# Optimization experiments

Hardware: AMD Instinct MI355X
Metric: run time of the kernel (lower is better)

Reference implementation:

```python
import jax, jax.numpy as jnp
import numpy as np

DIM_MODEL = 1024
NUM_HEADS = 16
DROPOUT_P = 0.5
SCALE = float(np.sqrt(DIM_MODEL // NUM_HEADS))  # NOTE: source MULTIPLIES by this (unusual but faithful)
DROP_KEY = jax.random.key(42)


def setup_inputs() -> dict:
    key = jax.random.key(0)
    ks = jax.random.split(key, 9)
    B, LQ, LK, D = 4, 2048, 2048, DIM_MODEL
    s = 1.0 / np.sqrt(D)
    return {
        "query": jax.random.normal(ks[0], (B, LQ, D), jnp.float32),
        "key": jax.random.normal(ks[1], (B, LK, D), jnp.float32),
        "value": jax.random.normal(ks[2], (B, LK, D), jnp.float32),
        "Wq": jax.random.normal(ks[3], (D, D), jnp.float32) * s,
        "bq": jax.random.normal(ks[4], (D,), jnp.float32) * s,
        "Wk": jax.random.normal(ks[5], (D, D), jnp.float32) * s,
        "bk": jax.random.normal(ks[6], (D,), jnp.float32) * s,
        "Wv": jax.random.normal(ks[7], (D, D), jnp.float32) * s,
        "bv": jax.random.normal(ks[8], (D,), jnp.float32) * s,
    }


def reference(query, key, value, Wq, bq, Wk, bk, Wv, bv):
    # Linear projections (W stored as [in, out])
    q = jnp.einsum('bqd,de->bqe', query, Wq) + bq
    k = jnp.einsum('bkd,de->bke', key, Wk) + bk
    v = jnp.einsum('bkd,de->bke', value, Wv) + bv
    # scores scaled by MULTIPLYING sqrt(d_head), per source
    scores = jnp.einsum('bqe,bke->bqk', q, k) * SCALE
    probs = jax.nn.softmax(scores, axis=-1)
    # dropout (train mode, p=0.5), deterministic fixed key for reproducibility
    keep = jax.random.bernoulli(DROP_KEY, 1.0 - DROPOUT_P, probs.shape)
    probs = jnp.where(keep, probs / (1.0 - DROPOUT_P), 0.0)
    return jnp.einsum('bqk,bke->bqe', probs, v)
```

## Files before the change

### kernel.cpp

```cpp
#include <hip/hip_runtime.h>
#include <math.h>

#define BATCH  4
#define LSEQ   2048
#define DMODEL 1024
#define MROWS  (BATCH * LSEQ)
#define SCORE_SCALE 8.0f

#define THREEFRY_PARTITIONABLE 1

typedef __bf16 bf16_t;
typedef bf16_t bf16x8 __attribute__((ext_vector_type(8)));
typedef bf16_t bf16x4 __attribute__((ext_vector_type(4)));
typedef float  f32x4  __attribute__((ext_vector_type(4)));

#define LDSP(p) ((__attribute__((address_space(3))) void*)(p))
#define GLBP(p) ((const __attribute__((address_space(1))) void*)(p))

__device__ __forceinline__ unsigned rotl32(unsigned x, int r) {
    return (x << r) | (x >> (32 - r));
}

__device__ __forceinline__ void threefry2x32(unsigned k0, unsigned k1,
                                             unsigned x0, unsigned x1,
                                             unsigned& o0, unsigned& o1) {
    const unsigned ks0 = k0, ks1 = k1, ks2 = k0 ^ k1 ^ 0x1BD11BDAu;
    x0 += ks0; x1 += ks1;
#define TF_R(r) { x0 += x1; x1 = rotl32(x1, r); x1 ^= x0; }
    TF_R(13) TF_R(15) TF_R(26) TF_R(6)
    x0 += ks1; x1 += ks2 + 1u;
    TF_R(17) TF_R(29) TF_R(16) TF_R(24)
    x0 += ks2; x1 += ks0 + 2u;
    TF_R(13) TF_R(15) TF_R(26) TF_R(6)
    x0 += ks0; x1 += ks1 + 3u;
    TF_R(17) TF_R(29) TF_R(16) TF_R(24)
    x0 += ks1; x1 += ks2 + 4u;
    TF_R(13) TF_R(15) TF_R(26) TF_R(6)
    x0 += ks2; x1 += ks0 + 5u;
#undef TF_R
    o0 = x0; o1 = x1;
}

__device__ __forceinline__ bool dropout_keep(unsigned n) {
    unsigned o0, o1;
#if THREEFRY_PARTITIONABLE
    threefry2x32(0u, 42u, 0u, n, o0, o1);
    unsigned bits = o0 ^ o1;
#else
    const unsigned HALF = (unsigned)(BATCH * LSEQ) * (unsigned)LSEQ / 2u;
    unsigned c0 = (n < HALF) ? n : (n - HALF);
    unsigned c1 = (n < HALF) ? (n + HALF) : n;
    threefry2x32(0u, 42u, c0, c1, o0, o1);
    unsigned bits = (n < HALF) ? o0 : o1;
#endif
    return bits < 0x80000000u;
}

__global__ __launch_bounds__(256)
void split_f32(const float* __restrict__ X0, const float* __restrict__ X1,
               bf16_t* __restrict__ hi, bf16_t* __restrict__ lo, int n) {
    const int y = blockIdx.y;
    const float* X = y ? X1 : X0;
    long long i = (long long)(blockIdx.x * 256 + threadIdx.x) * 4;
    if (i >= n) return;
    float4 v = *(const float4*)(X + i);
    bf16x4 h, l;
    h[0] = (bf16_t)v.x; l[0] = (bf16_t)(v.x - (float)h[0]);
    h[1] = (bf16_t)v.y; l[1] = (bf16_t)(v.y - (float)h[1]);
    h[2] = (bf16_t)v.z; l[2] = (bf16_t)(v.z - (float)h[2]);
    h[3] = (bf16_t)v.w; l[3] = (bf16_t)(v.w - (float)h[3]);
    *(bf16x4*)(hi + (long long)y * n + i) = h;
    *(bf16x4*)(lo + (long long)y * n + i) = l;
}

__global__ __launch_bounds__(256)
void split_transpose(const float* __restrict__ W0, const float* __restrict__ W1,
                     bf16_t* __restrict__ Th, bf16_t* __restrict__ Tl,
                     int Kd, int Nd) {
    __shared__ float t[32][33];
    const int z = blockIdx.z;
    const float* W = z ? W1 : W0;
    const long long zo = (long long)z * Kd * Nd;
    const int bx = blockIdx.x * 32;
    const int by = blockIdx.y * 32;
    const int tx = threadIdx.x & 31, ty = threadIdx.x >> 5;
#pragma unroll
    for (int i = 0; i < 4; ++i)
        t[ty + i * 8][tx] = W[(long long)(by + ty + i * 8) * Nd + bx + tx];
    __syncthreads();
#pragma unroll
    for (int i = 0; i < 4; ++i) {
        float v = t[tx][ty + i * 8];
        long long idx = zo + (long long)(bx + ty + i * 8) * Kd + by + tx;
        bf16_t h = (bf16_t)v;
        Th[idx] = h;
        Tl[idx] = (bf16_t)(v - (float)h);
    }
}

template <int SPLIT, int OUT, int BROW>
__global__ __launch_bounds__(256)
void gemm_mfma(const bf16_t* __restrict__ Ah, const bf16_t* __restrict__ Al,
               const bf16_t* __restrict__ Bh, const bf16_t* __restrict__ Bl,
               const float* __restrict__ bias, const float* __restrict__ bias2,
               float* __restrict__ Cf, bf16_t* __restrict__ Ch,
               bf16_t* __restrict__ Cl,
               int M, int N, int K, float scale,
               long long sA, long long sB, long long sC) {
    constexpr int TM = 128, TN = 128, TOT = 256, CHUNKS = 4;
    constexpr int NB = SPLIT ? 2 : 1;
    constexpr int BUFSZ = NB * TOT * 32;
    __shared__ __align__(16) bf16_t smem[2 * BUFSZ];

    const int tid = threadIdx.x;
    const int lane = tid & 63;
    const int wave = tid >> 6;
    const int quad = lane >> 4;
    const int l16 = lane & 15;
    const int wm = (wave & 1) * 64;
    const int wn = (wave >> 1) * 64;
    const long long z = blockIdx.z;
    const int m0 = blockIdx.y * TM, n0 = blockIdx.x * TN;

    const bf16_t* gAh = Ah + z * sA;
    const bf16_t* gBh = Bh + z * sB;
    const bf16_t* gAl = SPLIT ? Al + z * sA : nullptr;
    const bf16_t* gBl = SPLIT ? Bl + z * sB : nullptr;

    const int lrow = lane >> 2;
    const int scol = ((lane & 3) ^ ((lrow >> 1) & 3)) * 8;
    const int sw = (l16 >> 1) & 3;

    auto issue = [&](int k0, int b) {
        bf16_t* base = smem + b * BUFSZ;
#pragma unroll
        for (int c = 0; c < CHUNKS; ++c) {
            const int rbase = wave * 64 + c * 16;
            const int row = rbase + lrow;
            if (rbase < TM) {
                const long long g = (long long)(m0 + row) * K + k0 + scol;
                __builtin_amdgcn_global_load_lds(GLBP(gAh + g), LDSP(base + row * 32), 16, 0, 0);
                if constexpr (SPLIT)
                    __builtin_amdgcn_global_load_lds(GLBP(gAl + g), LDSP(base + TOT * 32 + row * 32), 16, 0, 0);
            } else {
                const int br = row - TM;
                const long long g = (long long)(n0 + br) * K + k0 + scol;
                __builtin_amdgcn_global_load_lds(GLBP(gBh + g), LDSP(base + TM * 32 + br * 32), 16, 0, 0);
                if constexpr (SPLIT)
                    __builtin_amdgcn_global_load_lds(GLBP(gBl + g), LDSP(base + TOT * 32 + TM * 32 + br * 32), 16, 0, 0);
            }
        }
    };

    f32x4 acc[4][4];
#pragma unroll
    for (int i = 0; i < 4; ++i)
#pragma unroll
        for (int j = 0; j < 4; ++j)
            acc[i][j] = (f32x4){0.f, 0.f, 0.f, 0.f};

    issue(0, 0);
    const int NIT = K >> 5;
    for (int it = 0; it < NIT; ++it) {
        const int b = it & 1;
        const bool more = (it + 1) < NIT;
        if (more) issue((it + 1) << 5, b ^ 1);
        if constexpr (SPLIT) {
            if (more) asm volatile("s_waitcnt vmcnt(8)" ::: "memory");
            else      asm volatile("s_waitcnt vmcnt(0)" ::: "memory");
        } else {
            if (more) asm volatile("s_waitcnt vmcnt(4)" ::: "memory");
            else      asm volatile("s_waitcnt vmcnt(0)" ::: "memory");
        }
        asm volatile("s_barrier" ::: "memory");

        bf16_t* base = smem + b * BUFSZ;
        bf16_t* sAh = base;
        bf16_t* sBh = base + TM * 32;
        bf16_t* sAl = base + TOT * 32;
        bf16_t* sBl = base + TOT * 32 + TM * 32;

        bf16x8 afh[4], bfh[4], afl[4], bfl[4];
#pragma unroll
        for (int i = 0; i < 4; ++i) {
            const int ao = (wm + i * 16 + l16) * 32 + (quad ^ sw) * 8;
            afh[i] = *(const bf16x8*)(sAh + ao);
            if constexpr (SPLIT) afl[i] = *(const bf16x8*)(sAl + ao);
        }
#pragma unroll
        for (int j = 0; j < 4; ++j) {
            const int bo = (wn + j * 16 + l16) * 32 + (quad ^ sw) * 8;
            bfh[j] = *(const bf16x8*)(sBh + bo);
            if constexpr (SPLIT) bfl[j] = *(const bf16x8*)(sBl + bo);
        }
#pragma unroll
        for (int i = 0; i < 4; ++i)
#pragma unroll
            for (int j = 0; j < 4; ++j) {
                acc[i][j] = __builtin_amdgcn_mfma_f32_16x16x32_bf16(afh[i], bfh[j], acc[i][j], 0, 0, 0);
                if constexpr (SPLIT) {
                    acc[i][j] = __builtin_amdgcn_mfma_f32_16x16x32_bf16(afh[i], bfl[j], acc[i][j], 0, 0, 0);
                    acc[i][j] = __builtin_amdgcn_mfma_f32_16x16x32_bf16(afl[i], bfh[j], acc[i][j], 0, 0, 0);
                }
            }
        asm volatile("s_barrier" ::: "memory");
    }

    const float* bz = (z == 1 && bias2) ? bias2 : bias;
#pragma unroll
    for (int i = 0; i < 4; ++i)
#pragma unroll
        for (int j = 0; j < 4; ++j) {
            const int n = n0 + wn + j * 16 + l16;
            float bvn = 0.f;
            if constexpr (OUT != 0 && !BROW) bvn = bz[n];
#pragma unroll
            for (int r = 0; r < 4; ++r) {
                const int m = m0 + wm + i * 16 + quad * 4 + r;
                const long long idx = z * sC + (long long)m * N + n;
                float v = acc[i][j][r];
                if constexpr (OUT == 0) {
                    Cf[idx] = v * scale;
                } else if constexpr (OUT == 1) {
                    v += bvn;
                    bf16_t h = (bf16_t)v;
                    Ch[idx] = h;
                    Cl[idx] = (bf16_t)(v - (float)h);
                } else {
                    v += BROW ? bz[m] : bvn;
                    Ch[idx] = (bf16_t)v;
                }
            }
        }
}

__global__ __launch_bounds__(256)
void softmax_dropout(const float* __restrict__ S, bf16_t* __restrict__ P) {
    const int LK = LSEQ;
    const unsigned row = blockIdx.x;
    const float* rowp = S + (long long)row * LK;
    bf16_t* prow = P + (long long)row * LK;
    __shared__ float buf[LSEQ];
    __shared__ float rbuf[256];
    const int tid = threadIdx.x;

    float m = -INFINITY;
    for (int j = tid; j < LK; j += 256) {
        float v = rowp[j];
        buf[j] = v;
        m = fmaxf(m, v);
    }
    rbuf[tid] = m;
    __syncthreads();
    for (int s = 128; s > 0; s >>= 1) {
        if (tid < s) rbuf[tid] = fmaxf(rbuf[tid], rbuf[tid + s]);
        __syncthreads();
    }
    m = rbuf[0];
    __syncthreads();

    float l = 0.f;
    for (int j = tid; j < LK; j += 256) {
        float e = expf(buf[j] - m);
        buf[j] = e;
        l += e;
    }
    rbuf[tid] = l;
    __syncthreads();
    for (int s = 128; s > 0; s >>= 1) {
        if (tid < s) rbuf[tid] += rbuf[tid + s];
        __syncthreads();
    }
    l = rbuf[0];

    const float inv = 2.0f / l;
    for (int j = tid; j < LK; j += 256) {
        unsigned n = row * (unsigned)LK + (unsigned)j;
        float p = dropout_keep(n) ? buf[j] * inv : 0.0f;
        prow[j] = (bf16_t)p;
    }
}

extern "C" void kernel_launch(void* const* d_in, const int* in_sizes, int n_in,
                              void* d_out, int out_size, void* d_ws, size_t ws_size,
                              hipStream_t stream) {
    const float* query = (const float*)d_in[0];
    const float* key_  = (const float*)d_in[1];
    const float* value = (const float*)d_in[2];
    const float* Wq = (const float*)d_in[3];
    const float* bq = (const float*)d_in[4];
    const float* Wk = (const float*)d_in[5];
    const float* bk = (const float*)d_in[6];
    const float* Wv = (const float*)d_in[7];
    const float* bv = (const float*)d_in[8];
    float* out = (float*)d_out;

    char* w = (char*)d_ws;
    const size_t Q1 = (size_t)MROWS * DMODEL * 2;
    bf16_t* Qh  = (bf16_t*)(w);
    bf16_t* Ql  = (bf16_t*)(w + 2 * Q1);
    bf16_t* VT  = (bf16_t*)(w + 4 * Q1);
    float*  S   = (float*)(w + 5 * Q1);
    bf16_t* XvH  = (bf16_t*)(w + 5 * Q1);
    bf16_t* XvL  = (bf16_t*)(w + 6 * Q1);
    bf16_t* XqkH = (bf16_t*)(w + 5 * Q1);
    bf16_t* XqkL = (bf16_t*)(w + 7 * Q1);
    bf16_t* WTh = (bf16_t*)(w + 9 * Q1);
    bf16_t* WTl = (bf16_t*)(w + 9 * Q1 + 2 * (size_t)DMODEL * DMODEL * 2);
    bf16_t* P   = Qh;

    dim3 b256(256);
    const int NELEM = MROWS * DMODEL;
    const long long DD = (long long)DMODEL * DMODEL;
    dim3 gwt1(DMODEL / 32, DMODEL / 32, 1);
    dim3 gwt2(DMODEL / 32, DMODEL / 32, 2);

    split_transpose<<<gwt1, b256, 0, stream>>>(Wv, nullptr, WTh, WTl, DMODEL, DMODEL);
    split_f32<<<dim3(NELEM / 1024, 1), b256, 0, stream>>>(value, nullptr, XvH, XvL, NELEM);
    gemm_mfma<0, 2, 1><<<dim3(LSEQ / 128, DMODEL / 128, BATCH), b256, 0, stream>>>(
        WTh, nullptr, XvH, nullptr, bv, nullptr, nullptr, VT, nullptr,
        DMODEL, LSEQ, DMODEL, 1.f,
        0, (long long)LSEQ * DMODEL, (long long)DMODEL * LSEQ);

    split_transpose<<<gwt2, b256, 0, stream>>>(Wq, Wk, WTh, WTl, DMODEL, DMODEL);
    split_f32<<<dim3(NELEM / 1024, 2), b256, 0, stream>>>(query, key_, XqkH, XqkL, NELEM);
    gemm_mfma<1, 1, 0><<<dim3(DMODEL / 128, MROWS / 128, 2), b256, 0, stream>>>(
        XqkH, XqkL, WTh, WTl, bq, bk, nullptr, Qh, Ql,
        MROWS, DMODEL, DMODEL, 1.f,
        (long long)NELEM, DD, (long long)NELEM);

    gemm_mfma<1, 0, 0><<<dim3(LSEQ / 128, LSEQ / 128, BATCH), b256, 0, stream>>>(
        Qh, Ql, Qh + NELEM, Ql + NELEM, nullptr, nullptr, S, nullptr, nullptr,
        LSEQ, LSEQ, DMODEL, SCORE_SCALE,
        (long long)LSEQ * DMODEL, (long long)LSEQ * DMODEL,
        (long long)LSEQ * LSEQ);

    softmax_dropout<<<dim3(MROWS), b256, 0, stream>>>(S, P);

    gemm_mfma<0, 0, 0><<<dim3(DMODEL / 128, LSEQ / 128, BATCH), b256, 0, stream>>>(
        P, nullptr, VT, nullptr, nullptr, nullptr, out, nullptr, nullptr,
        LSEQ, DMODEL, LSEQ, 1.f,
        (long long)LSEQ * LSEQ, (long long)DMODEL * LSEQ,
        (long long)LSEQ * DMODEL);
}
```

Measured before the change: 502.6 us.

## Remap GEMM blocks per XCD, register-resident softmax, single bf16 convert for value

GEMM launches become 1D grids, and the block index is decoded so that column tiles are grouped per XCD (bid&7). Blocks sharing an XCD's L2 then reuse the same operand panels. The softmax is rewritten to hold 8 elements per thread in registers, use wave shuffles for the reductions, use fast __expf, and write vectorized bf16 stores, removing the LDS buffer and tree-reduction barriers. The value input is now converted with a plain bf16 cast instead of the hi/lo split, since the lo half was unused, which saves writing a full buffer.

```diff
diff --git a/kernel.cpp b/kernel.cpp
--- a/kernel.cpp
+++ b/kernel.cpp
@@ -74,6 +74,18 @@
 }
 
 __global__ __launch_bounds__(256)
+void cvt_bf16(const float* __restrict__ X, bf16_t* __restrict__ Y, int n) {
+    long long i = (long long)(blockIdx.x * 256 + threadIdx.x) * 8;
+    if (i >= n) return;
+    float4 a = *(const float4*)(X + i);
+    float4 b = *(const float4*)(X + i + 4);
+    bf16x8 o;
+    o[0] = (bf16_t)a.x; o[1] = (bf16_t)a.y; o[2] = (bf16_t)a.z; o[3] = (bf16_t)a.w;
+    o[4] = (bf16_t)b.x; o[5] = (bf16_t)b.y; o[6] = (bf16_t)b.z; o[7] = (bf16_t)b.w;
+    *(bf16x8*)(Y + i) = o;
+}
+
+__global__ __launch_bounds__(256)
 void split_transpose(const float* __restrict__ W0, const float* __restrict__ W1,
                      bf16_t* __restrict__ Th, bf16_t* __restrict__ Tl,
                      int Kd, int Nd) {
@@ -106,11 +118,23 @@
                float* __restrict__ Cf, bf16_t* __restrict__ Ch,
                bf16_t* __restrict__ Cl,
                int M, int N, int K, float scale,
-               long long sA, long long sB, long long sC) {
+               long long sA, long long sB, long long sC,
+               int SX, int NYt) {
     constexpr int TM = 128, TN = 128, TOT = 256, CHUNKS = 4;
     constexpr int NB = SPLIT ? 2 : 1;
     constexpr int BUFSZ = NB * TOT * 32;
     __shared__ __align__(16) bf16_t smem[2 * BUFSZ];
+
+    const int bid = blockIdx.x;
+    const int xcd = bid & 7;
+    const int ii = bid >> 3;
+    const int perz = SX * NYt;
+    const int zz = ii / perz;
+    const int rr = ii - zz * perz;
+    const int nx = xcd + ((rr % SX) << 3);
+    const int my = rr / SX;
+    const long long z = zz;
+    const int m0 = my * TM, n0 = nx * TN;
 
     const int tid = threadIdx.x;
     const int lane = tid & 63;
@@ -119,8 +143,6 @@
     const int l16 = lane & 15;
     const int wm = (wave & 1) * 64;
     const int wn = (wave >> 1) * 64;
-    const long long z = blockIdx.z;
-    const int m0 = blockIdx.y * TM, n0 = blockIdx.x * TN;
 
     const bf16_t* gAh = Ah + z * sA;
     const bf16_t* gBh = Bh + z * sB;
@@ -236,49 +258,41 @@
 
 __global__ __launch_bounds__(256)
 void softmax_dropout(const float* __restrict__ S, bf16_t* __restrict__ P) {
-    const int LK = LSEQ;
     const unsigned row = blockIdx.x;
-    const float* rowp = S + (long long)row * LK;
-    bf16_t* prow = P + (long long)row * LK;
-    __shared__ float buf[LSEQ];
-    __shared__ float rbuf[256];
+    const float* rp = S + (long long)row * LSEQ;
     const int tid = threadIdx.x;
 
-    float m = -INFINITY;
-    for (int j = tid; j < LK; j += 256) {
-        float v = rowp[j];
-        buf[j] = v;
-        m = fmaxf(m, v);
-    }
-    rbuf[tid] = m;
+    float v[8];
+    *(float4*)(v)     = *(const float4*)(rp + tid * 8);
+    *(float4*)(v + 4) = *(const float4*)(rp + tid * 8 + 4);
+
+    float m = v[0];
+#pragma unroll
+    for (int e = 1; e < 8; ++e) m = fmaxf(m, v[e]);
+#pragma unroll
+    for (int o = 1; o < 64; o <<= 1) m = fmaxf(m, __shfl_xor(m, o));
+    __shared__ float redm[4];
+    if ((tid & 63) == 0) redm[tid >> 6] = m;
     __syncthreads();
-    for (int s = 128; s > 0; s >>= 1) {
-        if (tid < s) rbuf[tid] = fmaxf(rbuf[tid], rbuf[tid + s]);
-        __syncthreads();
-    }
-    m = rbuf[0];
+    m = fmaxf(fmaxf(redm[0], redm[1]), fmaxf(redm[2], redm[3]));
+
+    float s = 0.f;
+#pragma unroll
+    for (int e = 0; e < 8; ++e) { v[e] = __expf(v[e] - m); s += v[e]; }
+#pragma unroll
+    for (int o = 1; o < 64; o <<= 1) s += __shfl_xor(s, o);
+    __shared__ float reds[4];
+    if ((tid & 63) == 0) reds[tid >> 6] = s;
     __syncthreads();
-
-    float l = 0.f;
-    for (int j = tid; j < LK; j += 256) {
-        float e = expf(buf[j] - m);
-        buf[j] = e;
-        l += e;
-    }
-    rbuf[tid] = l;
-    __syncthreads();
-    for (int s = 128; s > 0; s >>= 1) {
-        if (tid < s) rbuf[tid] += rbuf[tid + s];
-        __syncthreads();
-    }
-    l = rbuf[0];
-
-    const float inv = 2.0f / l;
-    for (int j = tid; j < LK; j += 256) {
-        unsigned n = row * (unsigned)LK + (unsigned)j;
-        float p = dropout_keep(n) ? buf[j] * inv : 0.0f;
-        prow[j] = (bf16_t)p;
-    }
+    s = (reds[0] + reds[1]) + (reds[2] + reds[3]);
+
+    const float inv = 2.0f / s;
+    const unsigned nb = row * (unsigned)LSEQ + (unsigned)(tid * 8);
+    bf16x8 o8;
+#pragma unroll
+    for (int e = 0; e < 8; ++e)
+        o8[e] = (bf16_t)(dropout_keep(nb + e) ? v[e] * inv : 0.0f);
+    *(bf16x8*)(P + (long long)row * LSEQ + tid * 8) = o8;
 }
 
 extern "C" void kernel_launch(void* const* d_in, const int* in_sizes, int n_in,
@@ -302,7 +316,6 @@
     bf16_t* VT  = (bf16_t*)(w + 4 * Q1);
     float*  S   = (float*)(w + 5 * Q1);
     bf16_t* XvH  = (bf16_t*)(w + 5 * Q1);
-    bf16_t* XvL  = (bf16_t*)(w + 6 * Q1);
     bf16_t* XqkH = (bf16_t*)(w + 5 * Q1);
     bf16_t* XqkL = (bf16_t*)(w + 7 * Q1);
     bf16_t* WTh = (bf16_t*)(w + 9 * Q1);
@@ -316,30 +329,34 @@
     dim3 gwt2(DMODEL / 32, DMODEL / 32, 2);
 
     split_transpose<<<gwt1, b256, 0, stream>>>(Wv, nullptr, WTh, WTl, DMODEL, DMODEL);
-    split_f32<<<dim3(NELEM / 1024, 1), b256, 0, stream>>>(value, nullptr, XvH, XvL, NELEM);
-    gemm_mfma<0, 2, 1><<<dim3(LSEQ / 128, DMODEL / 128, BATCH), b256, 0, stream>>>(
+    cvt_bf16<<<dim3(NELEM / 2048), b256, 0, stream>>>(value, XvH, NELEM);
+    gemm_mfma<0, 2, 1><<<dim3(512), b256, 0, stream>>>(
         WTh, nullptr, XvH, nullptr, bv, nullptr, nullptr, VT, nullptr,
         DMODEL, LSEQ, DMODEL, 1.f,
-        0, (long long)LSEQ * DMODEL, (long long)DMODEL * LSEQ);
+        0, (long long)LSEQ * DMODEL, (long long)DMODEL * LSEQ,
+        2, DMODEL / 128);
 
     split_transpose<<<gwt2, b256, 0, stream>>>(Wq, Wk, WTh, WTl, DMODEL, DMODEL);
     split_f32<<<dim3(NELEM / 1024, 2), b256, 0, stream>>>(query, key_, XqkH, XqkL, NELEM);
-    gemm_mfma<1, 1, 0><<<dim3(DMODEL / 128, MROWS / 128, 2), b256, 0, stream>>>(
+    gemm_mfma<1, 1, 0><<<dim3(1024), b256, 0, stream>>>(
         XqkH, XqkL, WTh, WTl, bq, bk, nullptr, Qh, Ql,
         MROWS, DMODEL, DMODEL, 1.f,
-        (long long)NELEM, DD, (long long)NELEM);
-
-    gemm_mfma<1, 0, 0><<<dim3(LSEQ / 128, LSEQ / 128, BATCH), b256, 0, stream>>>(
+        (long long)NELEM, DD, (long long)NELEM,
+        1, MROWS / 128);
+
+    gemm_mfma<1, 0, 0><<<dim3(1024), b256, 0, stream>>>(
         Qh, Ql, Qh + NELEM, Ql + NELEM, nullptr, nullptr, S, nullptr, nullptr,
         LSEQ, LSEQ, DMODEL, SCORE_SCALE,
         (long long)LSEQ * DMODEL, (long long)LSEQ * DMODEL,
-        (long long)LSEQ * LSEQ);
+        (long long)LSEQ * LSEQ,
+        2, LSEQ / 128);
 
     softmax_dropout<<<dim3(MROWS), b256, 0, stream>>>(S, P);
 
-    gemm_mfma<0, 0, 0><<<dim3(DMODEL / 128, LSEQ / 128, BATCH), b256, 0, stream>>>(
+    gemm_mfma<0, 0, 0><<<dim3(512), b256, 0, stream>>>(
         P, nullptr, VT, nullptr, nullptr, nullptr, out, nullptr, nullptr,
         LSEQ, DMODEL, LSEQ, 1.f,
         (long long)LSEQ * LSEQ, (long long)DMODEL * LSEQ,
-        (long long)LSEQ * DMODEL);
-}
+        (long long)LSEQ * DMODEL,
+        1, LSEQ / 128);
+}
```

Result: faster. 477.1 us (-5.1%).
